# Performance work log

Measured on AMD Instinct MI355X. Metric: run time of the kernel, lower is better.

Reference implementation:

```python
import jax, jax.numpy as jnp
import numpy as np

B, SQ, SK, H = 8, 2048, 2048, 256
NH, HD = 4, 64  # num_heads, head_dim


def setup_inputs() -> dict:
    key = jax.random.key(0)
    ks = jax.random.split(key, 9)
    scale = 0.02
    inp = {
        'query': jax.random.normal(ks[0], (B, SQ, H), jnp.float32),
        'key':   jax.random.normal(ks[1], (B, SK, H), jnp.float32),
        'value': jax.random.normal(ks[2], (B, SK, H), jnp.float32),
        'mask':  jax.random.bernoulli(ks[3], 0.9, (B, SQ, SK)),
        'Wq': jax.random.normal(ks[4], (H, H), jnp.float32) * scale,
        'bq': jnp.zeros((H,), jnp.float32),
        'Wk': jax.random.normal(ks[5], (H, H), jnp.float32) * scale,
        'bk': jnp.zeros((H,), jnp.float32),
        'Wv': jax.random.normal(ks[6], (H, H), jnp.float32) * scale,
        'bv': jnp.zeros((H,), jnp.float32),
        'Wo': jax.random.normal(ks[7], (H, H), jnp.float32) * scale,
        'bo': jnp.zeros((H,), jnp.float32),
    }
    return inp


def reference(query, key, value, mask, Wq, bq, Wk, bk, Wv, bv, Wo, bo):
    b = query.shape[0]
    scale = jnp.asarray(HD, query.dtype) ** -0.5
    # torch Linear: x @ W.T + b; reshape to [B, NH, S, HD]
    Q = (query @ Wq.T + bq).reshape(b, -1, NH, HD).transpose(0, 2, 1, 3)
    K = (key   @ Wk.T + bk).reshape(b, -1, NH, HD).transpose(0, 2, 1, 3)
    V = (value @ Wv.T + bv).reshape(b, -1, NH, HD).transpose(0, 2, 1, 3)
    scores = jnp.einsum('bhqd,bhkd->bhqk', Q, K) * scale  # [B,NH,SQ,SK]
    # mask-fixing: rows with no valid key get key 0 unmasked
    mask_sum = mask.sum(axis=-1)  # [B,SQ]
    mask_fixed = mask.at[:, :, 0].set(jnp.where(mask_sum == 0, True, mask[:, :, 0]))
    scores = jnp.where(mask_fixed[:, None, :, :], scores, jnp.asarray(-1e9, scores.dtype))
    attn = jax.nn.softmax(scores, axis=-1)
    attn = jnp.where(jnp.isnan(attn), jnp.zeros_like(attn), attn)  # NaN fix
    out = jnp.einsum('bhqk,bhkd->bhqd', attn, V)
    out = out.transpose(0, 2, 1, 3).reshape(b, -1, H)
    out = out @ Wo.T + bo
    return out, attn
```

## Files before the change

kernel.cpp:

```cpp
#include <hip/hip_runtime.h>
#include <math.h>

#define Bn  8
#define SQn 2048
#define SKn 2048
#define Hn  256
#define NHn 4
#define HDn 64
#define SCALE2 0.1803368801111f

typedef __attribute__((ext_vector_type(4))) float f32x4;
typedef __attribute__((ext_vector_type(4))) unsigned int u32x4;
typedef __attribute__((ext_vector_type(8))) short short8;
typedef unsigned short ushort_t;
typedef unsigned long long ull_t;

__device__ __forceinline__ unsigned short f2bf(float f) {
  unsigned u = __builtin_bit_cast(unsigned, f);
  u += 0x7fffu + ((u >> 16) & 1u);
  return (unsigned short)(u >> 16);
}

__device__ __forceinline__ float fexp2(float x) {
  return __builtin_amdgcn_exp2f(x);
}

__device__ __forceinline__ short8 load8f(const float* p) {
  float4 v0 = *(const float4*)p;
  float4 v1 = *(const float4*)(p + 4);
  short8 r;
  r[0] = (short)f2bf(v0.x); r[1] = (short)f2bf(v0.y);
  r[2] = (short)f2bf(v0.z); r[3] = (short)f2bf(v0.w);
  r[4] = (short)f2bf(v1.x); r[5] = (short)f2bf(v1.y);
  r[6] = (short)f2bf(v1.z); r[7] = (short)f2bf(v1.w);
  return r;
}

__device__ __forceinline__ f32x4 mfma16(short8 a, short8 b, f32x4 c) {
  return __builtin_amdgcn_mfma_f32_16x16x32_bf16(a, b, c, 0, 0, 0);
}

__global__ __launch_bounds__(256) void maskbits_kernel(
    const void* __restrict__ maskp, ull_t* __restrict__ out)
{
  const int l = threadIdx.x & 63;
  const unsigned probe = ((const unsigned*)maskp)[l];
  const int isbyte = __any(probe > 1u);
  const int gwave = (blockIdx.x * 256 + threadIdx.x) >> 6;
  const int nwaves = gridDim.x * 4;
  const long long total = (long long)Bn * SQn * (SKn / 64);
  if (isbyte) {
    for (long long w = gwave; w < total; w += nwaves) {
      bool nz = ((const unsigned char*)maskp)[w * 64 + l] != 0;
      ull_t bal = __ballot(nz);
      if (l == 0) out[w] = bal;
    }
  } else {
    for (long long w = gwave; w < total; w += nwaves) {
      bool nz = ((const int*)maskp)[w * 64 + l] != 0;
      ull_t bal = __ballot(nz);
      if (l == 0) out[w] = bal;
    }
  }
}

__global__ __launch_bounds__(256) void proj3_kernel(
    const float* __restrict__ Xq, const float* __restrict__ Xk,
    const float* __restrict__ Xv,
    const float* __restrict__ Wqp, const float* __restrict__ bqp,
    const float* __restrict__ Wkp, const float* __restrict__ bkp,
    const float* __restrict__ Wvp, const float* __restrict__ bvp,
    ushort_t* __restrict__ Qb, ushort_t* __restrict__ Kb,
    ushort_t* __restrict__ Vt)
{
  const int which = blockIdx.z;
  const float* X = which == 0 ? Xq : which == 1 ? Xk : Xv;
  const float* W = which == 0 ? Wqp : which == 1 ? Wkp : Wvp;
  const float* bias = which == 0 ? bqp : which == 1 ? bkp : bvp;
  ushort_t* Y = which == 0 ? Qb : which == 1 ? Kb : Vt;
  const int vtrans = (which == 2);

  const int m0 = blockIdx.x * 64;
  const int n0 = blockIdx.y * 64;
  const int wv = threadIdx.x >> 6;
  const int l  = threadIdx.x & 63;
  const int lr = l & 15, lg = l >> 4;
  const int mrow = m0 + wv * 16 + lr;

  f32x4 acc[4];
  #pragma unroll
  for (int t = 0; t < 4; ++t) acc[t] = (f32x4){0.f, 0.f, 0.f, 0.f};

  const float* ap = X + (size_t)mrow * Hn + lg * 8;
  for (int k0 = 0; k0 < Hn; k0 += 32) {
    short8 a = load8f(ap + k0);
    #pragma unroll
    for (int t = 0; t < 4; ++t) {
      short8 bb = load8f(W + (size_t)(n0 + t * 16 + lr) * Hn + k0 + lg * 8);
      acc[t] = mfma16(a, bb, acc[t]);
    }
  }

  #pragma unroll
  for (int t = 0; t < 4; ++t) {
    const int n = n0 + t * 16 + lr;
    const float bv = bias[n];
    const int h = n >> 6, d = n & 63;
    if (!vtrans) {
      #pragma unroll
      for (int r = 0; r < 4; ++r) {
        const int m = m0 + wv * 16 + lg * 4 + r;
        const int bb = m >> 11, s = m & 2047;
        size_t idx = (((size_t)bb * NHn + h) * SQn + s) * HDn + d;
        Y[idx] = f2bf(acc[t][r] + bv);
      }
    } else {
      const int m = m0 + wv * 16 + lg * 4;
      const int bb = m >> 11, s = m & 2047;
      ushort4 pk;
      pk.x = f2bf(acc[t][0] + bv); pk.y = f2bf(acc[t][1] + bv);
      pk.z = f2bf(acc[t][2] + bv); pk.w = f2bf(acc[t][3] + bv);
      size_t idx = (((size_t)bb * NHn + h) * HDn + d) * (size_t)SKn + s;
      *(ushort4*)(Y + idx) = pk;
    }
  }
}

__global__ __launch_bounds__(512, 4) void fused_attn_kernel(
    const ushort_t* __restrict__ Qb, const ushort_t* __restrict__ Kb,
    const ushort_t* __restrict__ Vt, const unsigned* __restrict__ maskbits,
    float* __restrict__ attn_out, ushort_t* __restrict__ Ob)
{
  __shared__ float red[8][16];
  __shared__ float Opart[8][16][66];

  const int bid = blockIdx.x;
  const int rt = (bid & 7) * 512 + (bid >> 3);
  const int wv = threadIdx.x >> 6;
  const int l  = threadIdx.x & 63;
  const int lr = l & 15, lg = l >> 4;
  const int bh = rt >> 7;
  const int q0 = (rt & 127) << 4;
  const int b  = bh >> 2, h = bh & 3;
  const int colbase = wv * 256;

  const ushort_t* Qh = Qb + (size_t)bh * SQn * HDn;
  const ushort_t* Kh = Kb + (size_t)bh * SKn * HDn;
  const ushort_t* Vh = Vt + (size_t)bh * HDn * SKn;

  short8 qa0 = *(const short8*)(Qh + (q0 + lr) * HDn + lg * 8);
  short8 qa1 = *(const short8*)(Qh + (q0 + lr) * HDn + 32 + lg * 8);

  const int krA = (lr >> 2) * 8 + (lr & 3);
  const unsigned* mrow = maskbits + ((size_t)b * SQn + q0 + lr) * (SKn / 32) + wv * 8;
  u32x4 mwa = *(const u32x4*)mrow;
  u32x4 mwb = *(const u32x4*)(mrow + 4);
  const int bsh = lg * 8;

  float w[8][8];
  float lsum = 0.f;

  short8 ka0[2], ka1[2], kb0[2], kb1[2];
  {
    const ushort_t* kp = Kh + (size_t)(colbase + krA) * HDn + lg * 8;
    ka0[0] = *(const short8*)(kp);
    ka1[0] = *(const short8*)(kp + 32);
    kb0[0] = *(const short8*)(kp + 4 * HDn);
    kb1[0] = *(const short8*)(kp + 4 * HDn + 32);
  }
  #pragma unroll
  for (int s8 = 0; s8 < 8; ++s8) {
    const int cur = s8 & 1, nxt = cur ^ 1;
    if (s8 < 7) {
      const int cn = colbase + (s8 + 1) * 32;
      const ushort_t* kp = Kh + (size_t)(cn + krA) * HDn + lg * 8;
      ka0[nxt] = *(const short8*)(kp);
      ka1[nxt] = *(const short8*)(kp + 32);
      kb0[nxt] = *(const short8*)(kp + 4 * HDn);
      kb1[nxt] = *(const short8*)(kp + 4 * HDn + 32);
    }
    f32x4 za = (f32x4){0.f, 0.f, 0.f, 0.f}, zb = (f32x4){0.f, 0.f, 0.f, 0.f};
    za = mfma16(ka0[cur], qa0, za); za = mfma16(ka1[cur], qa1, za);
    zb = mfma16(kb0[cur], qa0, zb); zb = mfma16(kb1[cur], qa1, zb);

    const unsigned word = (s8 < 4) ? mwa[s8 & 3] : mwb[s8 & 3];
    const unsigned bits = (word >> bsh) & 0xFFu;
    #pragma unroll
    for (int j = 0; j < 4; ++j) {
      float pa = ((bits >> j) & 1) ? fexp2(za[j] * SCALE2) : 0.f;
      float pb = ((bits >> (4 + j)) & 1) ? fexp2(zb[j] * SCALE2) : 0.f;
      w[s8][j] = pa;
      w[s8][4 + j] = pb;
      lsum += pa + pb;
    }
  }

  lsum += __shfl_xor(lsum, 16);
  lsum += __shfl_xor(lsum, 32);
  if (l < 16) red[wv][lr] = lsum;
  __syncthreads();

  float gsum = 0.f;
  #pragma unroll
  for (int ww = 0; ww < 8; ++ww) gsum += red[ww][lr];
  const bool rowempty = (gsum == 0.f);
  const float rinv = rowempty ? 0.f : 1.f / gsum;

  float* arow = attn_out + ((size_t)bh * SQn + q0 + lr) * (size_t)SKn;
  f32x4 oacc[4];
  #pragma unroll
  for (int dt = 0; dt < 4; ++dt) oacc[dt] = (f32x4){0.f, 0.f, 0.f, 0.f};

  #pragma unroll
  for (int s8 = 0; s8 < 8; ++s8) {
    const int c = colbase + s8 * 32;
    const ushort_t* vp = Vh + (size_t)lr * SKn + c + lg * 8;
    short8 vb0 = *(const short8*)(vp);
    short8 vb1 = *(const short8*)(vp + 16 * SKn);
    short8 vb2 = *(const short8*)(vp + 32 * SKn);
    short8 vb3 = *(const short8*)(vp + 48 * SKn);

    float av[8];
    #pragma unroll
    for (int j = 0; j < 8; ++j) av[j] = w[s8][j] * rinv;
    if (rowempty && s8 == 0 && wv == 0 && lg == 0) av[0] = 1.f;

    __builtin_nontemporal_store((f32x4){av[0], av[1], av[2], av[3]},
                                (f32x4*)(arow + c + lg * 8));
    __builtin_nontemporal_store((f32x4){av[4], av[5], av[6], av[7]},
                                (f32x4*)(arow + c + lg * 8 + 4));

    short8 pf;
    #pragma unroll
    for (int j = 0; j < 8; ++j) pf[j] = (short)f2bf(av[j]);
    oacc[0] = mfma16(pf, vb0, oacc[0]);
    oacc[1] = mfma16(pf, vb1, oacc[1]);
    oacc[2] = mfma16(pf, vb2, oacc[2]);
    oacc[3] = mfma16(pf, vb3, oacc[3]);
  }

  #pragma unroll
  for (int dt = 0; dt < 4; ++dt)
    #pragma unroll
    for (int r = 0; r < 4; ++r)
      Opart[wv][lg * 4 + r][dt * 16 + lr] = oacc[dt][r];
  __syncthreads();

  #pragma unroll
  for (int e = threadIdx.x; e < 1024; e += 512) {
    const int row = e >> 6, d = e & 63;
    float s = 0.f;
    #pragma unroll
    for (int ww = 0; ww < 8; ++ww) s += Opart[ww][row][d];
    Ob[((size_t)b * SQn + q0 + row) * Hn + h * HDn + d] = f2bf(s);
  }
}

__global__ __launch_bounds__(256) void oproj_kernel(
    const unsigned short* __restrict__ A, const float* __restrict__ W,
    const float* __restrict__ bias, float* __restrict__ out)
{
  const int m0 = blockIdx.x * 64;
  const int n0 = blockIdx.y * 64;
  const int wv = threadIdx.x >> 6;
  const int l  = threadIdx.x & 63;
  const int lr = l & 15, lg = l >> 4;
  const int mrow = m0 + wv * 16 + lr;

  f32x4 acc[4];
  #pragma unroll
  for (int t = 0; t < 4; ++t) acc[t] = (f32x4){0.f, 0.f, 0.f, 0.f};

  for (int k0 = 0; k0 < Hn; k0 += 32) {
    short8 a = *(const short8*)(A + (size_t)mrow * Hn + k0 + lg * 8);
    #pragma unroll
    for (int t = 0; t < 4; ++t) {
      short8 bb = load8f(W + (size_t)(n0 + t * 16 + lr) * Hn + k0 + lg * 8);
      acc[t] = mfma16(a, bb, acc[t]);
    }
  }
  #pragma unroll
  for (int t = 0; t < 4; ++t) {
    const int n = n0 + t * 16 + lr;
    const float bv = bias[n];
    #pragma unroll
    for (int r = 0; r < 4; ++r) {
      const int m = m0 + wv * 16 + lg * 4 + r;
      out[(size_t)m * Hn + n] = acc[t][r] + bv;
    }
  }
}

extern "C" void kernel_launch(void* const* d_in, const int* in_sizes, int n_in,
                              void* d_out, int out_size, void* d_ws, size_t ws_size,
                              hipStream_t stream) {
  const float* query = (const float*)d_in[0];
  const float* key_  = (const float*)d_in[1];
  const float* value = (const float*)d_in[2];
  const void*  mask  = d_in[3];
  const float* Wq = (const float*)d_in[4];
  const float* bq = (const float*)d_in[5];
  const float* Wk = (const float*)d_in[6];
  const float* bk = (const float*)d_in[7];
  const float* Wv = (const float*)d_in[8];
  const float* bv = (const float*)d_in[9];
  const float* Wo = (const float*)d_in[10];
  const float* bo = (const float*)d_in[11];

  float* out  = (float*)d_out;
  float* attn = out + (size_t)Bn * SQn * Hn;

  char* ws = (char*)d_ws;
  unsigned short* Qb = (unsigned short*)ws;
  unsigned short* Kb = Qb + (size_t)Bn * SQn * Hn;
  unsigned short* Vt = Kb + (size_t)Bn * SKn * Hn;
  unsigned short* Ob = Vt + (size_t)Bn * SKn * Hn;
  unsigned* mbits = (unsigned*)(Ob + (size_t)Bn * SQn * Hn);

  maskbits_kernel<<<1024, 256, 0, stream>>>(mask, (ull_t*)mbits);
  proj3_kernel<<<dim3(256, 4, 3), 256, 0, stream>>>(
      query, key_, value, Wq, bq, Wk, bk, Wv, bv, Qb, Kb, Vt);
  fused_attn_kernel<<<4096, 512, 0, stream>>>(Qb, Kb, Vt, mbits, attn, Ob);
  oproj_kernel<<<dim3(256, 4), 256, 0, stream>>>(Ob, Wo, bo, out);
}
```

Before: 515.6 us.

## Fuse PV accumulation into score pass with deferred normalization

Moves the P·V MFMA accumulation into the first loop so it runs on unnormalized exp weights, and divides by the row sum only at the final reduction. The empty-row case is handled by writing V row 0 directly. This removes the second loop's V loads and bf16 conversions after the barrier, and drops one __syncthreads. It also replaces the K double-buffered prefetch with direct loads and sets waves_per_eu(4,4). In exchange, register pressure in the first loop rises and P is rounded to bf16 before normalization rather than after.

```diff
diff --git a/kernel.cpp b/kernel.cpp
--- a/kernel.cpp
+++ b/kernel.cpp
@@ -126,7 +126,9 @@
   }
 }
 
-__global__ __launch_bounds__(512, 4) void fused_attn_kernel(
+__global__ __launch_bounds__(512)
+__attribute__((amdgpu_waves_per_eu(4, 4)))
+void fused_attn_kernel(
     const ushort_t* __restrict__ Qb, const ushort_t* __restrict__ Kb,
     const ushort_t* __restrict__ Vt, const unsigned* __restrict__ maskbits,
     float* __restrict__ attn_out, ushort_t* __restrict__ Ob)
@@ -159,32 +161,31 @@
 
   float w[8][8];
   float lsum = 0.f;
-
-  short8 ka0[2], ka1[2], kb0[2], kb1[2];
-  {
-    const ushort_t* kp = Kh + (size_t)(colbase + krA) * HDn + lg * 8;
-    ka0[0] = *(const short8*)(kp);
-    ka1[0] = *(const short8*)(kp + 32);
-    kb0[0] = *(const short8*)(kp + 4 * HDn);
-    kb1[0] = *(const short8*)(kp + 4 * HDn + 32);
-  }
+  f32x4 oacc[4];
+  #pragma unroll
+  for (int dt = 0; dt < 4; ++dt) oacc[dt] = (f32x4){0.f, 0.f, 0.f, 0.f};
+
   #pragma unroll
   for (int s8 = 0; s8 < 8; ++s8) {
-    const int cur = s8 & 1, nxt = cur ^ 1;
-    if (s8 < 7) {
-      const int cn = colbase + (s8 + 1) * 32;
-      const ushort_t* kp = Kh + (size_t)(cn + krA) * HDn + lg * 8;
-      ka0[nxt] = *(const short8*)(kp);
-      ka1[nxt] = *(const short8*)(kp + 32);
-      kb0[nxt] = *(const short8*)(kp + 4 * HDn);
-      kb1[nxt] = *(const short8*)(kp + 4 * HDn + 32);
-    }
+    const int c = colbase + s8 * 32;
+    const ushort_t* kp = Kh + (size_t)(c + krA) * HDn + lg * 8;
+    short8 ka0 = *(const short8*)(kp);
+    short8 ka1 = *(const short8*)(kp + 32);
+    short8 kb0 = *(const short8*)(kp + 4 * HDn);
+    short8 kb1 = *(const short8*)(kp + 4 * HDn + 32);
     f32x4 za = (f32x4){0.f, 0.f, 0.f, 0.f}, zb = (f32x4){0.f, 0.f, 0.f, 0.f};
-    za = mfma16(ka0[cur], qa0, za); za = mfma16(ka1[cur], qa1, za);
-    zb = mfma16(kb0[cur], qa0, zb); zb = mfma16(kb1[cur], qa1, zb);
+    za = mfma16(ka0, qa0, za); za = mfma16(ka1, qa1, za);
+    zb = mfma16(kb0, qa0, zb); zb = mfma16(kb1, qa1, zb);
+
+    const ushort_t* vp = Vh + (size_t)lr * SKn + c + lg * 8;
+    short8 vb0 = *(const short8*)(vp);
+    short8 vb1 = *(const short8*)(vp + 16 * SKn);
+    short8 vb2 = *(const short8*)(vp + 32 * SKn);
+    short8 vb3 = *(const short8*)(vp + 48 * SKn);
 
     const unsigned word = (s8 < 4) ? mwa[s8 & 3] : mwb[s8 & 3];
     const unsigned bits = (word >> bsh) & 0xFFu;
+    short8 pf;
     #pragma unroll
     for (int j = 0; j < 4; ++j) {
       float pa = ((bits >> j) & 1) ? fexp2(za[j] * SCALE2) : 0.f;
@@ -192,12 +193,23 @@
       w[s8][j] = pa;
       w[s8][4 + j] = pb;
       lsum += pa + pb;
-    }
+      pf[j] = (short)f2bf(pa);
+      pf[4 + j] = (short)f2bf(pb);
+    }
+    oacc[0] = mfma16(pf, vb0, oacc[0]);
+    oacc[1] = mfma16(pf, vb1, oacc[1]);
+    oacc[2] = mfma16(pf, vb2, oacc[2]);
+    oacc[3] = mfma16(pf, vb3, oacc[3]);
   }
 
   lsum += __shfl_xor(lsum, 16);
   lsum += __shfl_xor(lsum, 32);
   if (l < 16) red[wv][lr] = lsum;
+  #pragma unroll
+  for (int dt = 0; dt < 4; ++dt)
+    #pragma unroll
+    for (int r = 0; r < 4; ++r)
+      Opart[wv][lg * 4 + r][dt * 16 + lr] = oacc[dt][r];
   __syncthreads();
 
   float gsum = 0.f;
@@ -207,52 +219,36 @@
   const float rinv = rowempty ? 0.f : 1.f / gsum;
 
   float* arow = attn_out + ((size_t)bh * SQn + q0 + lr) * (size_t)SKn;
-  f32x4 oacc[4];
-  #pragma unroll
-  for (int dt = 0; dt < 4; ++dt) oacc[dt] = (f32x4){0.f, 0.f, 0.f, 0.f};
-
   #pragma unroll
   for (int s8 = 0; s8 < 8; ++s8) {
     const int c = colbase + s8 * 32;
-    const ushort_t* vp = Vh + (size_t)lr * SKn + c + lg * 8;
-    short8 vb0 = *(const short8*)(vp);
-    short8 vb1 = *(const short8*)(vp + 16 * SKn);
-    short8 vb2 = *(const short8*)(vp + 32 * SKn);
-    short8 vb3 = *(const short8*)(vp + 48 * SKn);
-
     float av[8];
     #pragma unroll
     for (int j = 0; j < 8; ++j) av[j] = w[s8][j] * rinv;
     if (rowempty && s8 == 0 && wv == 0 && lg == 0) av[0] = 1.f;
-
     __builtin_nontemporal_store((f32x4){av[0], av[1], av[2], av[3]},
                                 (f32x4*)(arow + c + lg * 8));
     __builtin_nontemporal_store((f32x4){av[4], av[5], av[6], av[7]},
                                 (f32x4*)(arow + c + lg * 8 + 4));
-
-    short8 pf;
-    #pragma unroll
-    for (int j = 0; j < 8; ++j) pf[j] = (short)f2bf(av[j]);
-    oacc[0] = mfma16(pf, vb0, oacc[0]);
-    oacc[1] = mfma16(pf, vb1, oacc[1]);
-    oacc[2] = mfma16(pf, vb2, oacc[2]);
-    oacc[3] = mfma16(pf, vb3, oacc[3]);
-  }
-
-  #pragma unroll
-  for (int dt = 0; dt < 4; ++dt)
-    #pragma unroll
-    for (int r = 0; r < 4; ++r)
-      Opart[wv][lg * 4 + r][dt * 16 + lr] = oacc[dt][r];
-  __syncthreads();
+  }
 
   #pragma unroll
   for (int e = threadIdx.x; e < 1024; e += 512) {
     const int row = e >> 6, d = e & 63;
+    float gs = 0.f;
+    #pragma unroll
+    for (int ww = 0; ww < 8; ++ww) gs += red[ww][row];
     float s = 0.f;
     #pragma unroll
     for (int ww = 0; ww < 8; ++ww) s += Opart[ww][row][d];
-    Ob[((size_t)b * SQn + q0 + row) * Hn + h * HDn + d] = f2bf(s);
+    float val;
+    if (gs == 0.f) {
+      unsigned u = (unsigned)Vh[(size_t)d * SKn] << 16;
+      val = __builtin_bit_cast(float, u);
+    } else {
+      val = s / gs;
+    }
+    Ob[((size_t)b * SQn + q0 + row) * Hn + h * HDn + d] = f2bf(val);
   }
 }
 
```

New measurement: 523.4 us. Within noise of the previous version (+1.5%).
